# Optimization experiments

Hardware: AMD Instinct MI355X
Metric: run time of the kernel (lower is better)

## Reference

```python
import jax, jax.numpy as jnp
import numpy as np

B = 512      # streamlines (graphs in the batch)
L = 128      # points per streamline
M = L - 1    # edges per direction per streamline == conv output length
IN = 3       # 3-D coordinates
K = 5        # kNN neighbors (self included, as in PyG knn)
FOV = 5      # conv kernel; odd so conv out length == M, matching the batch vector
PAD = FOV // 2
NC = 2
EPS = 1e-5


def _bn(x, g, b, m, v):
    # inference-mode BatchNorm1d
    return (x - m) * jax.lax.rsqrt(v + EPS) * g + b


def setup_inputs():
    key = jax.random.key(0)
    ks = jax.random.split(key, 20)
    r = lambda i, shape: jax.random.normal(ks[i], shape, jnp.float32) * 0.05
    ones = lambda n: jnp.ones((n,), jnp.float32)
    zeros = lambda n: jnp.zeros((n,), jnp.float32)
    pos = jax.random.normal(ks[0], (B * L, IN), jnp.float32)
    # consecutive-point (forward) edges, streamline-major order
    base = (jnp.arange(B)[:, None] * L + jnp.arange(M)[None, :]).reshape(-1)
    fwd = jnp.stack([base, base + 1]).astype(jnp.int32)          # [2, B*M]
    eidx = jnp.concatenate([fwd, fwd], axis=1)                   # [2, 2*B*M]; first half overwritten in forward
    batch = jnp.repeat(jnp.arange(B, dtype=jnp.int32), L)        # per-point graph id
    lengths = jnp.full((B,), L, dtype=jnp.int32)
    return dict(
        pos=pos, eidx=eidx, batch=batch, lengths=lengths,
        conv1_w=r(1, (FOV, 2 * IN, 64)), conv1_b=r(2, (64,)),
        bn1_g=ones(64), bn1_b=zeros(64), bn1_m=r(3, (64,)), bn1_v=ones(64),
        edge_w=r(4, (2 * 64, 128)), edge_b=r(5, (128,)),
        bn2_g=ones(128), bn2_b=zeros(128), bn2_m=r(6, (128,)), bn2_v=ones(128),
        lin1_w=r(7, (64 + 128, 1024)), lin1_b=r(8, (1024,)),
        bn3_g=ones(1024), bn3_b=zeros(1024), bn3_m=r(9, (1024,)), bn3_v=ones(1024),
        m1_w=r(10, (1024, 512)), m1_b=r(11, (512,)),
        bn4_g=ones(512), bn4_b=zeros(512), bn4_m=r(12, (512,)), bn4_v=ones(512),
        m2_w=r(13, (512, 256)), m2_b=r(14, (256,)),
        bn5_g=ones(256), bn5_b=zeros(256), bn5_m=r(15, (256,)), bn5_v=ones(256),
        out_w=r(16, (256, NC)), out_b=r(17, (NC,)),
    )


def reference(pos, eidx, batch, lengths,
              conv1_w, conv1_b, bn1_g, bn1_b, bn1_m, bn1_v,
              edge_w, edge_b, bn2_g, bn2_b, bn2_m, bn2_v,
              lin1_w, lin1_b, bn3_g, bn3_b, bn3_m, bn3_v,
              m1_w, m1_b, bn4_g, bn4_b, bn4_m, bn4_v,
              m2_w, m2_b, bn5_g, bn5_b, bn5_m, bn5_v,
              out_w, out_b):
    E = eidx.shape[1]
    half = eidx[:, E // 2:]
    # eidx[:, :E//2] = eidx[:, E//2:].flip(1)
    eidx = jnp.concatenate([half[:, ::-1], half], axis=1)
    # irregular gather: edge features [E, 2*IN]
    feats = jnp.concatenate([pos[eidx[1]] - pos[eidx[0]], pos[eidx[0]]], axis=1)
    x = feats.reshape(2 * B, M, 2 * IN)                            # folded direction+batch
    # Conv1d (cross-correlation) -> BN -> ReLU, channels-last layout
    x = jax.lax.conv_general_dilated(x, conv1_w, (1,), [(PAD, PAD)],
                                     dimension_numbers=('NWC', 'WIO', 'NWC')) + conv1_b
    x = jax.nn.relu(_bn(x, bn1_g, bn1_b, bn1_m, bn1_v))            # [2B, M, 64]
    # direction symmetrization: max(first half, second half flipped on batch & length)
    x = jnp.maximum(x[:B], x[B:][::-1, ::-1, :])                   # [B, M, 64]
    x1 = x.reshape(B * M, 64)
    # ---- DynamicEdgeConv: per-streamline kNN graph + edge MLP + max aggregation ----
    xg = x1.reshape(B, M, 64)
    sq = jnp.sum(xg * xg, axis=-1)                                 # [B, M]
    dist = sq[:, :, None] + sq[:, None, :] - 2.0 * jnp.einsum('bmd,bnd->bmn', xg, xg)
    _, idx = jax.lax.top_k(-dist, K)                               # [B, M, K] (self included)
    xj = jax.vmap(lambda xs, ix: xs[ix])(xg, idx)                  # [B, M, K, 64]
    xi = jnp.broadcast_to(xg[:, :, None, :], xj.shape)
    ef = jnp.concatenate([xi, xj - xi], axis=-1)                   # [B, M, K, 128]
    ef = _bn(jax.nn.relu(ef @ edge_w + edge_b), bn2_g, bn2_b, bn2_m, bn2_v)
    x2 = jnp.max(ef, axis=2).reshape(B * M, 128)                   # max aggr over neighbors
    # ---- lin1 + global max pool + classifier MLP (dropout = identity in eval) ----
    h = jnp.concatenate([x1, x2], axis=1)                          # [N, 192]
    h = _bn(jax.nn.relu(h @ lin1_w + lin1_b), bn3_g, bn3_b, bn3_m, bn3_v)  # [N, 1024]
    g = jnp.max(h.reshape(B, M, 1024), axis=1)                     # global_max_pool -> [B, 1024]
    g = _bn(jax.nn.relu(g @ m1_w + m1_b), bn4_g, bn4_b, bn4_m, bn4_v)
    g = _bn(jax.nn.relu(g @ m2_w + m2_b), bn5_g, bn5_b, bn5_m, bn5_v)
    return g @ out_w + out_b                                       # [B, NC]
```

## Files before the change

### kernel.cpp

```cpp
#include <hip/hip_runtime.h>

#define BB 512
#define LL 128
#define MM 127
#define EPS 1e-5f

typedef _Float16 half4 __attribute__((ext_vector_type(4)));
typedef _Float16 half8 __attribute__((ext_vector_type(8)));
typedef float f32x16 __attribute__((ext_vector_type(16)));

#define HB_PITCH 384
#define HB_BATCH 49152

__global__ __launch_bounds__(256) void k0_prep(
    const float* __restrict__ lw, char* __restrict__ lwT,
    const float* __restrict__ ew, char* __restrict__ ewT,
    const float* __restrict__ m1w, char* __restrict__ m1wT,
    const float* __restrict__ m2w, char* __restrict__ m2wT)
{
  int tid = threadIdx.x;
  __shared__ float ws2[256][32];
  if (blockIdx.x < 32) {
    int c0 = blockIdx.x * 32;
    __shared__ float wcol[192][32];
    for (int i = tid; i < 192 * 32; i += 256) {
      int k = i >> 5, c = i & 31;
      wcol[k][c] = lw[k * 1024 + c0 + c];
    }
    __syncthreads();
    for (int j = tid; j < 768; j += 256) {
      int kg = j >> 5, c = j & 31;
      half8 v;
#pragma unroll
      for (int jj = 0; jj < 8; jj++) v[jj] = (_Float16)wcol[kg * 8 + jj][c];
      int cc = c0 + c;
      *(half8*)(lwT + cc * HB_PITCH + ((kg * 16) ^ ((cc & 7) << 4))) = v;
    }
  } else if (blockIdx.x == 32) {
    __shared__ float es[128][128];
    for (int i = tid; i < 128 * 128; i += 256) es[i >> 7][i & 127] = ew[i];
    __syncthreads();
    for (int i = tid; i < 256 * 8; i += 256) {
      int c = i >> 3, kg = i & 7;
      half8 v;
#pragma unroll
      for (int jj = 0; jj < 8; jj++) {
        int k = kg * 8 + jj;
        float val = (c < 128) ? (es[k][c] - es[64 + k][c]) : es[64 + k][c - 128];
        v[jj] = (_Float16)val;
      }
      *(half8*)(ewT + c * 128 + ((kg * 16) ^ ((c & 7) << 4))) = v;
    }
  } else {
    const float* src; char* dst; int N, K, c0, k0;
    if (blockIdx.x < 97) {
      int bb = blockIdx.x - 33;
      src = m1w; dst = m1wT; N = 512; K = 1024;
      c0 = (bb >> 2) * 32; k0 = (bb & 3) * 256;
    } else {
      int bb = blockIdx.x - 97;
      src = m2w; dst = m2wT; N = 256; K = 512;
      c0 = (bb >> 1) * 32; k0 = (bb & 1) * 256;
    }
    for (int i = tid; i < 256 * 32; i += 256) {
      int k = i >> 5, c = i & 31;
      ws2[k][c] = src[(size_t)(k0 + k) * N + c0 + c];
    }
    __syncthreads();
    for (int j = tid; j < 32 * 32; j += 256) {
      int kg = j >> 5, c = j & 31;
      half8 v;
#pragma unroll
      for (int jj = 0; jj < 8; jj++) v[jj] = (_Float16)ws2[kg * 8 + jj][c];
      int cc = c0 + c;
      *(half8*)(dst + (size_t)cc * (2 * K) + ((2 * (k0 + kg * 8)) ^ ((cc & 7) << 4))) = v;
    }
  }
}

__global__ __launch_bounds__(512, 2) void k1_conv_knn(
    const float* __restrict__ pos, const float* __restrict__ cw,
    const float* __restrict__ cb, const float* __restrict__ g1,
    const float* __restrict__ b1, const float* __restrict__ m1,
    const float* __restrict__ v1, char* __restrict__ hb,
    int* __restrict__ idxb)
{
  int b = blockIdx.x;
  int tid = threadIdx.x;
  __shared__ float fpad[132][8];
  __shared__ float xs[128][64];
  __shared__ float sq[128];
  __shared__ float S[128][132];
  __shared__ float bsl[4][128][5];
  __shared__ int   bil[4][128][5];

  if (tid < 40) {
    int rr = tid >> 3;
    int row = (rr < 2) ? rr : (127 + rr);
    fpad[row][tid & 7] = 0.f;
  }
  if (tid < 64) xs[127][tid] = 0.f;
  const float* pb = pos + b * LL * 3;
  for (int i = tid; i < MM * 6; i += 512) {
    int m = i / 6, c = i % 6;
    float v = (c < 3) ? (pb[(m + 1) * 3 + c] - pb[m * 3 + c]) : pb[m * 3 + c - 3];
    fpad[m + 2][c] = v;
  }
  int orow = BB - 1 - b;
  char* hbb = hb + (size_t)orow * HB_BATCH;
  if (tid < 8) *(float4*)(hbb + 127 * HB_PITCH + tid * 16) = make_float4(0.f, 0.f, 0.f, 0.f);

  int c = tid & 63, cg = tid >> 6;
  float wreg[30];
#pragma unroll
  for (int t = 0; t < 5; t++)
#pragma unroll
    for (int ci = 0; ci < 6; ci++) wreg[t * 6 + ci] = cw[(t * 6 + ci) * 64 + c];
  float s1 = g1[c] * rsqrtf(v1[c] + EPS);
  float t1 = (cb[c] - m1[c]) * s1 + b1[c];
  __syncthreads();

#pragma unroll
  for (int it = 0; it < 4; it++) {
    int chunk = cg + 8 * it;
    int m0 = chunk * 4;
    float4 fa[8], fb[8];
#pragma unroll
    for (int r = 0; r < 8; r++) {
      fa[r] = *(const float4*)&fpad[m0 + r][0];
      fb[r] = *(const float4*)&fpad[m0 + r][4];
    }
#pragma unroll
    for (int mm = 0; mm < 4; mm++) {
      int m = m0 + mm;
      if (m >= MM) continue;
      float af = 0.f, ab = 0.f;
#pragma unroll
      for (int t = 0; t < 5; t++) {
#pragma unroll
        for (int ci = 0; ci < 6; ci++) {
          float w = wreg[t * 6 + ci];
          int rf = mm + t, rb = mm + 4 - t;
          float xf = (ci < 4) ? ((const float*)&fa[rf])[ci] : ((const float*)&fb[rf])[ci - 4];
          float xb = (ci < 4) ? ((const float*)&fa[rb])[ci] : ((const float*)&fb[rb])[ci - 4];
          af = fmaf(xf, w, af);
          ab = fmaf(xb, w, ab);
        }
      }
      float z = fmaxf(af, ab) * s1 + t1;
      float xv = fmaxf(z, 0.f);
      int p = MM - 1 - m;
      xs[p][(((c >> 2) + (p >> 3)) & 15) * 4 + (c & 3)] = xv;
      *(_Float16*)(hbb + p * HB_PITCH + ((2 * c) ^ ((p & 7) << 4))) = (_Float16)xv;
    }
  }
  __syncthreads();
  if (tid < 128) {
    int r = tid;
    float s = 0.f;
#pragma unroll
    for (int c4 = 0; c4 < 16; c4++) {
      float4 v = *(const float4*)&xs[r][((c4 + (r >> 3)) & 15) * 4];
      s = fmaf(v.x, v.x, s); s = fmaf(v.y, v.y, s);
      s = fmaf(v.z, v.z, s); s = fmaf(v.w, v.w, s);
    }
    sq[r] = s;
  }
  __syncthreads();
  if (tid < 256) {
    int tr = tid >> 4, tc = tid & 15;
    float acc[8][8];
#pragma unroll
    for (int i = 0; i < 8; i++)
#pragma unroll
      for (int j = 0; j < 8; j++) acc[i][j] = 0.f;
    for (int k4 = 0; k4 < 16; k4++) {
      int ca = ((k4 + tr) & 15) * 4;
      int cbo = ((k4 + tc) & 15) * 4;
      float4 av[8], bv[8];
#pragma unroll
      for (int i = 0; i < 8; i++) av[i] = *(const float4*)&xs[tr * 8 + i][ca];
#pragma unroll
      for (int j = 0; j < 8; j++) bv[j] = *(const float4*)&xs[tc * 8 + j][cbo];
#pragma unroll
      for (int i = 0; i < 8; i++)
#pragma unroll
        for (int j = 0; j < 8; j++) {
          acc[i][j] = fmaf(av[i].x, bv[j].x, acc[i][j]);
          acc[i][j] = fmaf(av[i].y, bv[j].y, acc[i][j]);
          acc[i][j] = fmaf(av[i].z, bv[j].z, acc[i][j]);
          acc[i][j] = fmaf(av[i].w, bv[j].w, acc[i][j]);
        }
    }
    float sqc[8];
#pragma unroll
    for (int j = 0; j < 8; j++) sqc[j] = sq[tc * 8 + j];
#pragma unroll
    for (int i = 0; i < 8; i++) {
      float4 s0, s1v;
      s0.x = sqc[0] - 2.f * acc[i][0]; s0.y = sqc[1] - 2.f * acc[i][1];
      s0.z = sqc[2] - 2.f * acc[i][2]; s0.w = sqc[3] - 2.f * acc[i][3];
      s1v.x = sqc[4] - 2.f * acc[i][4]; s1v.y = sqc[5] - 2.f * acc[i][5];
      s1v.z = sqc[6] - 2.f * acc[i][6]; s1v.w = sqc[7] - 2.f * acc[i][7];
      *(float4*)&S[tr * 8 + i][tc * 8]     = s0;
      *(float4*)&S[tr * 8 + i][tc * 8 + 4] = s1v;
    }
  }
  __syncthreads();
  {
    int row = tid & 127, q = tid >> 7;
    float bs[5]; int bi[5];
#pragma unroll
    for (int k = 0; k < 5; k++) { bs[k] = 1e30f; bi[k] = 0; }
#pragma unroll
    for (int e4 = 0; e4 < 8; e4++) {
      float4 sv = *(const float4*)&S[row][q * 32 + e4 * 4];
      int cbase = q * 32 + e4 * 4;
      float va[4] = {sv.x, sv.y, sv.z, sv.w};
#pragma unroll
      for (int e = 0; e < 4; e++) {
        int col = cbase + e;
        float sc = va[e];
        if (col < 127 && sc < bs[4]) {
          bs[4] = sc; bi[4] = col;
#pragma unroll
          for (int k = 3; k >= 0; k--) {
            if (bs[k + 1] < bs[k]) {
              float ts = bs[k]; bs[k] = bs[k + 1]; bs[k + 1] = ts;
              int ti = bi[k]; bi[k] = bi[k + 1]; bi[k + 1] = ti;
            }
          }
        }
      }
    }
#pragma unroll
    for (int k = 0; k < 5; k++) { bsl[q][row][k] = bs[k]; bil[q][row][k] = bi[k]; }
  }
  __syncthreads();
  if (tid < MM) {
    int i0 = 0, i1 = 0, i2 = 0, i3 = 0;
    int base = (orow * MM + tid) * 5;
#pragma unroll
    for (int k = 0; k < 5; k++) {
      float v0 = bsl[0][tid][i0], v1 = bsl[1][tid][i1];
      float v2 = bsl[2][tid][i2], v3 = bsl[3][tid][i3];
      float best = v0; int q = 0;
      if (v1 < best) { best = v1; q = 1; }
      if (v2 < best) { best = v2; q = 2; }
      if (v3 < best) { best = v3; q = 3; }
      int iq = (q == 0) ? i0 : (q == 1) ? i1 : (q == 2) ? i2 : i3;
      idxb[base + k] = bil[q][tid][iq];
      if (q == 0) i0++; else if (q == 1) i1++; else if (q == 2) i2++; else i3++;
    }
  }
}

__global__ __launch_bounds__(256) void k3_edge(
    const int* __restrict__ idxb, const char* __restrict__ ewT,
    const float* __restrict__ eb, const float* __restrict__ g2,
    const float* __restrict__ b2, const float* __restrict__ m2,
    const float* __restrict__ v2, char* __restrict__ hb)
{
  int b = blockIdx.x;
  int tid = threadIdx.x;
  int w = tid >> 6, l = tid & 63;
  int lo = l & 31, hi = l >> 5;
  __shared__ _Float16 vvs[MM][136];
  __shared__ int idxs[MM * 5];
  char* hbb = hb + (size_t)b * HB_BATCH;

  for (int i = tid; i < MM * 5; i += 256) idxs[i] = idxb[b * MM * 5 + i];
  if (tid < 16) *(float4*)(hbb + 127 * HB_PITCH + 128 + tid * 16) = make_float4(0.f, 0.f, 0.f, 0.f);

  half8 af[4][4];
#pragma unroll
  for (int rt = 0; rt < 4; rt++) {
    int row = rt * 32 + lo;
    const char* rb = hbb + row * HB_PITCH;
    int sz = (row & 7) << 4;
#pragma unroll
    for (int ks = 0; ks < 4; ks++)
      af[rt][ks] = *(const half8*)(rb + ((ks * 32 + hi * 16) ^ sz));
  }
  int cu = w * 32 + lo;
  int swzW = (cu & 7) << 4;
  const char* wu = ewT + cu * 128;
  const char* wv = ewT + (128 + cu) * 128;
  half8 bu[4], bv[4];
#pragma unroll
  for (int ks = 0; ks < 4; ks++) {
    int off = (ks * 32 + hi * 16) ^ swzW;
    bu[ks] = *(const half8*)(wu + off);
    bv[ks] = *(const half8*)(wv + off);
  }
  f32x16 accu[4], accv[4];
#pragma unroll
  for (int rt = 0; rt < 4; rt++)
#pragma unroll
    for (int r = 0; r < 16; r++) { accu[rt][r] = 0.f; accv[rt][r] = 0.f; }
#pragma unroll
  for (int ks = 0; ks < 4; ks++)
#pragma unroll
    for (int rt = 0; rt < 4; rt++) {
      accu[rt] = __builtin_amdgcn_mfma_f32_32x32x16_f16(af[rt][ks], bu[ks], accu[rt], 0, 0, 0);
      accv[rt] = __builtin_amdgcn_mfma_f32_32x32x16_f16(af[rt][ks], bv[ks], accv[rt], 0, 0, 0);
    }
#pragma unroll
  for (int rt = 0; rt < 4; rt++)
#pragma unroll
    for (int r = 0; r < 16; r++) {
      int p = rt * 32 + (r & 3) + 8 * (r >> 2) + 4 * hi;
      if (p < MM) vvs[p][cu] = (_Float16)accv[rt][r];
    }
  __syncthreads();
  float ebv = eb[cu];
  float s2 = g2[cu] * rsqrtf(v2[cu] + EPS);
  float t2 = b2[cu] - m2[cu] * s2;
#pragma unroll
  for (int rt = 0; rt < 4; rt++)
#pragma unroll
    for (int r = 0; r < 16; r++) {
      int p = rt * 32 + (r & 3) + 8 * (r >> 2) + 4 * hi;
      if (p >= MM) continue;
      const int* ip = &idxs[p * 5];
      float u = accu[rt][r];
      float mx = -1e30f;
#pragma unroll
      for (int k = 0; k < 5; k++)
        mx = fmaxf(mx, u + (float)vvs[ip[k]][cu]);
      float o = fmaxf(mx + ebv, 0.f) * s2 + t2;
      *(_Float16*)(hbb + p * HB_PITCH + ((128 + 2 * cu) ^ ((p & 7) << 4))) = (_Float16)o;
    }
}

__global__ __launch_bounds__(512, 2) void k4_lin1(
    const char* __restrict__ hb, const char* __restrict__ lwT,
    const float* __restrict__ lb, const float* __restrict__ g3,
    const float* __restrict__ b3, const float* __restrict__ m3,
    const float* __restrict__ v3, char* __restrict__ gbufh)
{
  int b = blockIdx.x;
  int tid = threadIdx.x;
  int w = tid >> 6;
  int rh = w >> 2, cq = w & 3;
  int l = tid & 63;
  int lo = l & 31, hi = l >> 5;
  __shared__ __align__(16) char sA[HB_BATCH];
  __shared__ float rmslab[2][1024];

  {
    const char* gA = hb + (size_t)b * HB_BATCH;
#pragma unroll
    for (int i = 0; i < 6; i++)
      *(float4*)(sA + (i * 512 + tid) * 16) = *(const float4*)(gA + (i * 512 + tid) * 16);
  }
  __syncthreads();

  int sz = (lo & 7) << 4;
  half8 af[2][12];
#pragma unroll
  for (int q = 0; q < 2; q++) {
    const char* rbase = sA + ((rh * 2 + q) * 32 + lo) * HB_PITCH;
#pragma unroll
    for (int ks = 0; ks < 12; ks++)
      af[q][ks] = *(const half8*)(rbase + ((ks * 32 + hi * 16) ^ sz));
  }

  int col0 = cq * 256 + lo;
  half8 bf[2][12];
  {
    const char* cb0 = lwT + (size_t)col0 * HB_PITCH;
#pragma unroll
    for (int ks = 0; ks < 12; ks++)
      bf[0][ks] = *(const half8*)(cb0 + ((ks * 32 + hi * 16) ^ sz));
  }
#pragma unroll
  for (int ct = 0; ct < 8; ct++) {
    if (ct < 7) {
      const char* cbn = lwT + (size_t)(col0 + (ct + 1) * 32) * HB_PITCH;
#pragma unroll
      for (int ks = 0; ks < 12; ks++)
        bf[(ct + 1) & 1][ks] = *(const half8*)(cbn + ((ks * 32 + hi * 16) ^ sz));
    }
    f32x16 acc[2];
#pragma unroll
    for (int q = 0; q < 2; q++)
#pragma unroll
      for (int r = 0; r < 16; r++) acc[q][r] = 0.f;
#pragma unroll
    for (int ks = 0; ks < 12; ks++) {
      acc[0] = __builtin_amdgcn_mfma_f32_32x32x16_f16(af[0][ks], bf[ct & 1][ks], acc[0], 0, 0, 0);
      acc[1] = __builtin_amdgcn_mfma_f32_32x32x16_f16(af[1][ks], bf[ct & 1][ks], acc[1], 0, 0, 0);
    }
    int col = col0 + ct * 32;
    float bias = lb[col];
    float rm = 0.f;
#pragma unroll
    for (int q = 0; q < 2; q++)
#pragma unroll
      for (int r = 0; r < 16; r++) {
        float v = fmaxf(acc[q][r] + bias, 0.f);
        if (q == 1 && r == 15) v = (rh == 1 && hi == 1) ? 0.f : v;
        rm = fmaxf(rm, v);
      }
    rm = fmaxf(rm, __shfl_xor(rm, 32));
    if (hi == 0) rmslab[rh][col] = rm;
  }
  __syncthreads();
  if (tid < 256) {
    half4 o;
#pragma unroll
    for (int j = 0; j < 4; j++) {
      int c = tid * 4 + j;
      float mv = fmaxf(rmslab[0][c], rmslab[1][c]);
      float s = g3[c] * rsqrtf(v3[c] + EPS);
      float t = b3[c] - m3[c] * s;
      o[j] = (_Float16)(mv * s + t);
    }
    *(half4*)(gbufh + (size_t)b * 2048 + ((8 * tid) ^ ((b & 7) << 4))) = o;
  }
}

template<int K, int N>
__global__ __launch_bounds__(64) void k5_gemm(
    const char* __restrict__ inh, const char* __restrict__ wT,
    const float* __restrict__ bias, const float* __restrict__ gg,
    const float* __restrict__ bbp, const float* __restrict__ mmp,
    const float* __restrict__ vvp, char* __restrict__ outh,
    float* __restrict__ outf)
{
  constexpr int NT = N / 32;
  constexpr int NC = K / 128;
  int bid = blockIdx.x;
  int mt = bid / NT, nt = bid % NT;
  int l = threadIdx.x;
  int lo = l & 31, hi = l >> 5;
  int row = mt * 32 + lo, col = nt * 32 + lo;
  const char* arow = inh + (size_t)row * (2 * K);
  const char* brow = wT + (size_t)col * (2 * K);
  int sza = (row & 7) << 4, szb = (col & 7) << 4;

  half8 a[2][8], bf[2][8];
#pragma unroll
  for (int ks = 0; ks < 8; ks++) {
    int off = ks * 32 + hi * 16;
    a[0][ks]  = *(const half8*)(arow + (off ^ sza));
    bf[0][ks] = *(const half8*)(brow + (off ^ szb));
  }
  f32x16 acc;
#pragma unroll
  for (int r = 0; r < 16; r++) acc[r] = 0.f;
#pragma unroll
  for (int c = 0; c < NC; c++) {
    if (c + 1 < NC) {
#pragma unroll
      for (int ks = 0; ks < 8; ks++) {
        int off = (c + 1) * 256 + ks * 32 + hi * 16;
        a[(c + 1) & 1][ks]  = *(const half8*)(arow + (off ^ sza));
        bf[(c + 1) & 1][ks] = *(const half8*)(brow + (off ^ szb));
      }
    }
#pragma unroll
    for (int ks = 0; ks < 8; ks++)
      acc = __builtin_amdgcn_mfma_f32_32x32x16_f16(a[c & 1][ks], bf[c & 1][ks], acc, 0, 0, 0);
  }
  float bv = bias[col];
  float s = gg[col] * rsqrtf(vvp[col] + EPS);
  float t = bbp[col] - mmp[col] * s;
#pragma unroll
  for (int r = 0; r < 16; r++) {
    float z = fmaxf(acc[r] + bv, 0.f) * s + t;
    int orow = mt * 32 + (r & 3) + 8 * (r >> 2) + 4 * hi;
    if (outh)
      *(_Float16*)(outh + (size_t)orow * (2 * N) + ((2 * col) ^ ((orow & 7) << 4))) = (_Float16)z;
    else
      outf[(size_t)orow * N + col] = z;
  }
}

__global__ __launch_bounds__(256) void k5c_out(
    const float* __restrict__ c2, const float* __restrict__ ow,
    const float* __restrict__ ob, float* __restrict__ out)
{
  int t = blockIdx.x * 256 + threadIdx.x;
  int r = t >> 1, c = t & 1;
  float acc = 0.f;
  for (int d4 = 0; d4 < 64; d4++) {
    float4 cv = *(const float4*)(c2 + r * 256 + d4 * 4);
    acc = fmaf(cv.x, ow[(d4 * 4 + 0) * 2 + c], acc);
    acc = fmaf(cv.y, ow[(d4 * 4 + 1) * 2 + c], acc);
    acc = fmaf(cv.z, ow[(d4 * 4 + 2) * 2 + c], acc);
    acc = fmaf(cv.w, ow[(d4 * 4 + 3) * 2 + c], acc);
  }
  out[t] = acc + ob[c];
}

extern "C" void kernel_launch(void* const* d_in, const int* in_sizes, int n_in,
                              void* d_out, int out_size, void* d_ws, size_t ws_size,
                              hipStream_t stream)
{
  const float* pos = (const float*)d_in[0];
  const float* cw  = (const float*)d_in[4];
  const float* cb  = (const float*)d_in[5];
  const float* g1  = (const float*)d_in[6];
  const float* b1  = (const float*)d_in[7];
  const float* m1  = (const float*)d_in[8];
  const float* v1  = (const float*)d_in[9];
  const float* ew  = (const float*)d_in[10];
  const float* eb  = (const float*)d_in[11];
  const float* g2  = (const float*)d_in[12];
  const float* b2  = (const float*)d_in[13];
  const float* m2  = (const float*)d_in[14];
  const float* v2  = (const float*)d_in[15];
  const float* lw  = (const float*)d_in[16];
  const float* lb  = (const float*)d_in[17];
  const float* g3  = (const float*)d_in[18];
  const float* b3  = (const float*)d_in[19];
  const float* m3  = (const float*)d_in[20];
  const float* v3  = (const float*)d_in[21];
  const float* m1w = (const float*)d_in[22];
  const float* m1b = (const float*)d_in[23];
  const float* g4  = (const float*)d_in[24];
  const float* b4  = (const float*)d_in[25];
  const float* m4  = (const float*)d_in[26];
  const float* v4  = (const float*)d_in[27];
  const float* m2w = (const float*)d_in[28];
  const float* m2b = (const float*)d_in[29];
  const float* g5  = (const float*)d_in[30];
  const float* b5  = (const float*)d_in[31];
  const float* m5  = (const float*)d_in[32];
  const float* v5  = (const float*)d_in[33];
  const float* ow  = (const float*)d_in[34];
  const float* ob  = (const float*)d_in[35];

  char* ws = (char*)d_ws;
  char*  hb    = ws;
  char*  lwT   = ws + 25165824;
  char*  ewT   = ws + 25559040;
  int*   idxb  = (int*)(ws + 25591808);
  char*  gbufh = ws + 26892288;
  char*  m1wT  = ws + 27940864;
  char*  c1h   = ws + 28989440;
  char*  m2wT  = ws + 29513728;
  float* c2    = (float*)(ws + 29775872);

  hipLaunchKernelGGL(k0_prep, dim3(113), dim3(256), 0, stream,
                     lw, lwT, ew, ewT, m1w, m1wT, m2w, m2wT);
  hipLaunchKernelGGL(k1_conv_knn, dim3(512), dim3(512), 0, stream,
                     pos, cw, cb, g1, b1, m1, v1, hb, idxb);
  hipLaunchKernelGGL(k3_edge, dim3(512), dim3(256), 0, stream,
                     idxb, ewT, eb, g2, b2, m2, v2, hb);
  hipLaunchKernelGGL(k4_lin1, dim3(512), dim3(512), 0, stream,
                     hb, lwT, lb, g3, b3, m3, v3, gbufh);
  (k5_gemm<1024, 512>)<<<dim3(256), dim3(64), 0, stream>>>(
      gbufh, m1wT, m1b, g4, b4, m4, v4, c1h, nullptr);
  (k5_gemm<512, 256>)<<<dim3(128), dim3(64), 0, stream>>>(
      c1h, m2wT, m2b, g5, b5, m5, v5, nullptr, c2);
  hipLaunchKernelGGL(k5c_out, dim3(4), dim3(256), 0, stream,
                     c2, ow, ob, (float*)d_out);
}
```

Measured before the change: 128.3 us.

## Shrink kNN kernel to 256 threads and two-pass distance tiles in smaller LDS

The conv+kNN kernel now runs with 256 threads per block instead of 512. The 128x128 distance matrix is computed in two 64-column halves, written to a 128x68 scratch buffer that aliases the conv input padding. A single thread per row streams both halves through one running top-5 list, which removes the four-way partial lists and their merge. Shared memory per block drops a lot, so more blocks can be resident. In exchange, only 128 threads do the selection scan, and it adds an extra barrier per pass.

```diff
diff --git a/kernel.cpp b/kernel.cpp
--- a/kernel.cpp
+++ b/kernel.cpp
@@ -78,7 +78,7 @@
   }
 }
 
-__global__ __launch_bounds__(512, 2) void k1_conv_knn(
+__global__ __launch_bounds__(256, 2) void k1_conv_knn(
     const float* __restrict__ pos, const float* __restrict__ cw,
     const float* __restrict__ cb, const float* __restrict__ g1,
     const float* __restrict__ b1, const float* __restrict__ m1,
@@ -87,12 +87,10 @@
 {
   int b = blockIdx.x;
   int tid = threadIdx.x;
-  __shared__ float fpad[132][8];
   __shared__ float xs[128][64];
   __shared__ float sq[128];
-  __shared__ float S[128][132];
-  __shared__ float bsl[4][128][5];
-  __shared__ int   bil[4][128][5];
+  __shared__ __align__(16) float Sbuf[128][68];
+  float (*fpad)[8] = (float(*)[8])Sbuf;
 
   if (tid < 40) {
     int rr = tid >> 3;
@@ -101,7 +99,7 @@
   }
   if (tid < 64) xs[127][tid] = 0.f;
   const float* pb = pos + b * LL * 3;
-  for (int i = tid; i < MM * 6; i += 512) {
+  for (int i = tid; i < MM * 6; i += 256) {
     int m = i / 6, c = i % 6;
     float v = (c < 3) ? (pb[(m + 1) * 3 + c] - pb[m * 3 + c]) : pb[m * 3 + c - 3];
     fpad[m + 2][c] = v;
@@ -121,8 +119,8 @@
   __syncthreads();
 
 #pragma unroll
-  for (int it = 0; it < 4; it++) {
-    int chunk = cg + 8 * it;
+  for (int it = 0; it < 8; it++) {
+    int chunk = cg + 4 * it;
     int m0 = chunk * 4;
     float4 fa[8], fb[8];
 #pragma unroll
@@ -167,91 +165,84 @@
     sq[r] = s;
   }
   __syncthreads();
-  if (tid < 256) {
-    int tr = tid >> 4, tc = tid & 15;
-    float acc[8][8];
-#pragma unroll
-    for (int i = 0; i < 8; i++)
-#pragma unroll
-      for (int j = 0; j < 8; j++) acc[i][j] = 0.f;
-    for (int k4 = 0; k4 < 16; k4++) {
-      int ca = ((k4 + tr) & 15) * 4;
-      int cbo = ((k4 + tc) & 15) * 4;
-      float4 av[8], bv[8];
-#pragma unroll
-      for (int i = 0; i < 8; i++) av[i] = *(const float4*)&xs[tr * 8 + i][ca];
-#pragma unroll
-      for (int j = 0; j < 8; j++) bv[j] = *(const float4*)&xs[tc * 8 + j][cbo];
+
+  float bs[5]; int bi[5];
+#pragma unroll
+  for (int k = 0; k < 5; k++) { bs[k] = 1e30f; bi[k] = 0; }
+  int tr = tid >> 4, tc = tid & 15;
+
+#pragma unroll
+  for (int pass = 0; pass < 2; pass++) {
+    {
+      int j0 = pass * 64 + tc * 4;
+      int jb = pass * 8 + (tc >> 1);
+      float acc[8][4];
 #pragma unroll
       for (int i = 0; i < 8; i++)
 #pragma unroll
-        for (int j = 0; j < 8; j++) {
-          acc[i][j] = fmaf(av[i].x, bv[j].x, acc[i][j]);
-          acc[i][j] = fmaf(av[i].y, bv[j].y, acc[i][j]);
-          acc[i][j] = fmaf(av[i].z, bv[j].z, acc[i][j]);
-          acc[i][j] = fmaf(av[i].w, bv[j].w, acc[i][j]);
-        }
-    }
-    float sqc[8];
-#pragma unroll
-    for (int j = 0; j < 8; j++) sqc[j] = sq[tc * 8 + j];
-#pragma unroll
-    for (int i = 0; i < 8; i++) {
-      float4 s0, s1v;
-      s0.x = sqc[0] - 2.f * acc[i][0]; s0.y = sqc[1] - 2.f * acc[i][1];
-      s0.z = sqc[2] - 2.f * acc[i][2]; s0.w = sqc[3] - 2.f * acc[i][3];
-      s1v.x = sqc[4] - 2.f * acc[i][4]; s1v.y = sqc[5] - 2.f * acc[i][5];
-      s1v.z = sqc[6] - 2.f * acc[i][6]; s1v.w = sqc[7] - 2.f * acc[i][7];
-      *(float4*)&S[tr * 8 + i][tc * 8]     = s0;
-      *(float4*)&S[tr * 8 + i][tc * 8 + 4] = s1v;
-    }
-  }
-  __syncthreads();
-  {
-    int row = tid & 127, q = tid >> 7;
-    float bs[5]; int bi[5];
-#pragma unroll
-    for (int k = 0; k < 5; k++) { bs[k] = 1e30f; bi[k] = 0; }
-#pragma unroll
-    for (int e4 = 0; e4 < 8; e4++) {
-      float4 sv = *(const float4*)&S[row][q * 32 + e4 * 4];
-      int cbase = q * 32 + e4 * 4;
-      float va[4] = {sv.x, sv.y, sv.z, sv.w};
-#pragma unroll
-      for (int e = 0; e < 4; e++) {
-        int col = cbase + e;
-        float sc = va[e];
-        if (col < 127 && sc < bs[4]) {
-          bs[4] = sc; bi[4] = col;
-#pragma unroll
-          for (int k = 3; k >= 0; k--) {
-            if (bs[k + 1] < bs[k]) {
-              float ts = bs[k]; bs[k] = bs[k + 1]; bs[k + 1] = ts;
-              int ti = bi[k]; bi[k] = bi[k + 1]; bi[k + 1] = ti;
+        for (int j = 0; j < 4; j++) acc[i][j] = 0.f;
+      for (int k4 = 0; k4 < 16; k4++) {
+        int ca = ((k4 + tr) & 15) * 4;
+        int cbo = ((k4 + jb) & 15) * 4;
+        float4 av[8], bv[4];
+#pragma unroll
+        for (int i = 0; i < 8; i++) av[i] = *(const float4*)&xs[tr * 8 + i][ca];
+#pragma unroll
+        for (int j = 0; j < 4; j++) bv[j] = *(const float4*)&xs[j0 + j][cbo];
+#pragma unroll
+        for (int i = 0; i < 8; i++)
+#pragma unroll
+          for (int j = 0; j < 4; j++) {
+            acc[i][j] = fmaf(av[i].x, bv[j].x, acc[i][j]);
+            acc[i][j] = fmaf(av[i].y, bv[j].y, acc[i][j]);
+            acc[i][j] = fmaf(av[i].z, bv[j].z, acc[i][j]);
+            acc[i][j] = fmaf(av[i].w, bv[j].w, acc[i][j]);
+          }
+      }
+      float sqc[4];
+#pragma unroll
+      for (int j = 0; j < 4; j++) sqc[j] = sq[j0 + j];
+#pragma unroll
+      for (int i = 0; i < 8; i++) {
+        float4 s0;
+        s0.x = sqc[0] - 2.f * acc[i][0];
+        s0.y = sqc[1] - 2.f * acc[i][1];
+        s0.z = sqc[2] - 2.f * acc[i][2];
+        s0.w = sqc[3] - 2.f * acc[i][3];
+        *(float4*)&Sbuf[tr * 8 + i][tc * 4] = s0;
+      }
+    }
+    __syncthreads();
+    if (tid < 128) {
+      int row = tid;
+#pragma unroll
+      for (int e4 = 0; e4 < 16; e4++) {
+        float4 sv = *(const float4*)&Sbuf[row][e4 * 4];
+        int cbase = pass * 64 + e4 * 4;
+        float va[4] = {sv.x, sv.y, sv.z, sv.w};
+#pragma unroll
+        for (int e = 0; e < 4; e++) {
+          int col = cbase + e;
+          float sc = va[e];
+          if (col < 127 && sc < bs[4]) {
+            bs[4] = sc; bi[4] = col;
+#pragma unroll
+            for (int k = 3; k >= 0; k--) {
+              if (bs[k + 1] < bs[k]) {
+                float ts = bs[k]; bs[k] = bs[k + 1]; bs[k + 1] = ts;
+                int ti = bi[k]; bi[k] = bi[k + 1]; bi[k + 1] = ti;
+              }
             }
           }
         }
       }
     }
-#pragma unroll
-    for (int k = 0; k < 5; k++) { bsl[q][row][k] = bs[k]; bil[q][row][k] = bi[k]; }
-  }
-  __syncthreads();
+    __syncthreads();
+  }
   if (tid < MM) {
-    int i0 = 0, i1 = 0, i2 = 0, i3 = 0;
     int base = (orow * MM + tid) * 5;
 #pragma unroll
-    for (int k = 0; k < 5; k++) {
-      float v0 = bsl[0][tid][i0], v1 = bsl[1][tid][i1];
-      float v2 = bsl[2][tid][i2], v3 = bsl[3][tid][i3];
-      float best = v0; int q = 0;
-      if (v1 < best) { best = v1; q = 1; }
-      if (v2 < best) { best = v2; q = 2; }
-      if (v3 < best) { best = v3; q = 3; }
-      int iq = (q == 0) ? i0 : (q == 1) ? i1 : (q == 2) ? i2 : i3;
-      idxb[base + k] = bil[q][tid][iq];
-      if (q == 0) i0++; else if (q == 1) i1++; else if (q == 2) i2++; else i3++;
-    }
+    for (int k = 0; k < 5; k++) idxb[base + k] = bi[k];
   }
 }
 
@@ -546,7 +537,7 @@
 
   hipLaunchKernelGGL(k0_prep, dim3(113), dim3(256), 0, stream,
                      lw, lwT, ew, ewT, m1w, m1wT, m2w, m2wT);
-  hipLaunchKernelGGL(k1_conv_knn, dim3(512), dim3(512), 0, stream,
+  hipLaunchKernelGGL(k1_conv_knn, dim3(512), dim3(256), 0, stream,
                      pos, cw, cb, g1, b1, m1, v1, hb, idxb);
   hipLaunchKernelGGL(k3_edge, dim3(512), dim3(256), 0, stream,
                      idxb, ewT, eb, g2, b2, m2, v2, hb);
```

Result: slower. 159.3 us (+24.1%).

## Split fused conv+kNN kernel into conv and half-row kNN kernels

Applied to the files above, without the earlier changes.

The fused conv1+kNN kernel is split in two. The first kernel runs the conv and writes its fp32 features to a global scratch buffer. The second kernel runs kNN over 1024 blocks, each handling half the query rows of one streamline, so the distance computation and top-k get more parallelism and each block uses less shared memory. The cost is an extra kernel launch, a global round-trip for the features, and recomputing the squared norms in both halves.

```diff
diff --git a/kernel.cpp b/kernel.cpp
--- a/kernel.cpp
+++ b/kernel.cpp
@@ -78,37 +78,33 @@
   }
 }
 
-__global__ __launch_bounds__(512, 2) void k1_conv_knn(
+__global__ __launch_bounds__(256) void k1a_conv(
     const float* __restrict__ pos, const float* __restrict__ cw,
     const float* __restrict__ cb, const float* __restrict__ g1,
     const float* __restrict__ b1, const float* __restrict__ m1,
     const float* __restrict__ v1, char* __restrict__ hb,
-    int* __restrict__ idxb)
+    float* __restrict__ xgr)
 {
   int b = blockIdx.x;
   int tid = threadIdx.x;
   __shared__ float fpad[132][8];
-  __shared__ float xs[128][64];
-  __shared__ float sq[128];
-  __shared__ float S[128][132];
-  __shared__ float bsl[4][128][5];
-  __shared__ int   bil[4][128][5];
 
   if (tid < 40) {
     int rr = tid >> 3;
     int row = (rr < 2) ? rr : (127 + rr);
     fpad[row][tid & 7] = 0.f;
   }
-  if (tid < 64) xs[127][tid] = 0.f;
   const float* pb = pos + b * LL * 3;
-  for (int i = tid; i < MM * 6; i += 512) {
+  for (int i = tid; i < MM * 6; i += 256) {
     int m = i / 6, c = i % 6;
     float v = (c < 3) ? (pb[(m + 1) * 3 + c] - pb[m * 3 + c]) : pb[m * 3 + c - 3];
     fpad[m + 2][c] = v;
   }
   int orow = BB - 1 - b;
   char* hbb = hb + (size_t)orow * HB_BATCH;
+  float* xgb = xgr + (size_t)orow * 8192;
   if (tid < 8) *(float4*)(hbb + 127 * HB_PITCH + tid * 16) = make_float4(0.f, 0.f, 0.f, 0.f);
+  if (tid < 16) *(float4*)(xgb + 127 * 64 + tid * 4) = make_float4(0.f, 0.f, 0.f, 0.f);
 
   int c = tid & 63, cg = tid >> 6;
   float wreg[30];
@@ -121,8 +117,8 @@
   __syncthreads();
 
 #pragma unroll
-  for (int it = 0; it < 4; it++) {
-    int chunk = cg + 8 * it;
+  for (int it = 0; it < 8; it++) {
+    int chunk = cg + 4 * it;
     int m0 = chunk * 4;
     float4 fa[8], fb[8];
 #pragma unroll
@@ -150,10 +146,27 @@
       float z = fmaxf(af, ab) * s1 + t1;
       float xv = fmaxf(z, 0.f);
       int p = MM - 1 - m;
-      xs[p][(((c >> 2) + (p >> 3)) & 15) * 4 + (c & 3)] = xv;
+      xgb[p * 64 + (((c >> 2) + (p >> 3)) & 15) * 4 + (c & 3)] = xv;
       *(_Float16*)(hbb + p * HB_PITCH + ((2 * c) ^ ((p & 7) << 4))) = (_Float16)xv;
     }
   }
+}
+
+__global__ __launch_bounds__(256, 2) void k1b_knn(
+    const float* __restrict__ xgr, int* __restrict__ idxb)
+{
+  int bid = blockIdx.x;
+  int ob = bid >> 1, hf = bid & 1;
+  int r0 = hf * 64;
+  int tid = threadIdx.x;
+  __shared__ float xs[128][64];
+  __shared__ float sq[128];
+  __shared__ float S[64][132];
+  __shared__ float bsl[4][64][5];
+  __shared__ int   bil[4][64][5];
+
+  const float4* src = (const float4*)(xgr + (size_t)ob * 8192);
+  for (int i = tid; i < 2048; i += 256) ((float4*)xs)[i] = src[i];
   __syncthreads();
   if (tid < 128) {
     int r = tid;
@@ -167,23 +180,25 @@
     sq[r] = s;
   }
   __syncthreads();
-  if (tid < 256) {
+  {
     int tr = tid >> 4, tc = tid & 15;
-    float acc[8][8];
-#pragma unroll
-    for (int i = 0; i < 8; i++)
+    int ra = r0 + tr * 4;
+    int ga = ra >> 3;
+    float acc[4][8];
+#pragma unroll
+    for (int i = 0; i < 4; i++)
 #pragma unroll
       for (int j = 0; j < 8; j++) acc[i][j] = 0.f;
     for (int k4 = 0; k4 < 16; k4++) {
-      int ca = ((k4 + tr) & 15) * 4;
+      int ca = ((k4 + ga) & 15) * 4;
       int cbo = ((k4 + tc) & 15) * 4;
-      float4 av[8], bv[8];
-#pragma unroll
-      for (int i = 0; i < 8; i++) av[i] = *(const float4*)&xs[tr * 8 + i][ca];
+      float4 av[4], bv[8];
+#pragma unroll
+      for (int i = 0; i < 4; i++) av[i] = *(const float4*)&xs[ra + i][ca];
 #pragma unroll
       for (int j = 0; j < 8; j++) bv[j] = *(const float4*)&xs[tc * 8 + j][cbo];
 #pragma unroll
-      for (int i = 0; i < 8; i++)
+      for (int i = 0; i < 4; i++)
 #pragma unroll
         for (int j = 0; j < 8; j++) {
           acc[i][j] = fmaf(av[i].x, bv[j].x, acc[i][j]);
@@ -196,19 +211,19 @@
 #pragma unroll
     for (int j = 0; j < 8; j++) sqc[j] = sq[tc * 8 + j];
 #pragma unroll
-    for (int i = 0; i < 8; i++) {
+    for (int i = 0; i < 4; i++) {
       float4 s0, s1v;
       s0.x = sqc[0] - 2.f * acc[i][0]; s0.y = sqc[1] - 2.f * acc[i][1];
       s0.z = sqc[2] - 2.f * acc[i][2]; s0.w = sqc[3] - 2.f * acc[i][3];
       s1v.x = sqc[4] - 2.f * acc[i][4]; s1v.y = sqc[5] - 2.f * acc[i][5];
       s1v.z = sqc[6] - 2.f * acc[i][6]; s1v.w = sqc[7] - 2.f * acc[i][7];
-      *(float4*)&S[tr * 8 + i][tc * 8]     = s0;
-      *(float4*)&S[tr * 8 + i][tc * 8 + 4] = s1v;
+      *(float4*)&S[tr * 4 + i][tc * 8]     = s0;
+      *(float4*)&S[tr * 4 + i][tc * 8 + 4] = s1v;
     }
   }
   __syncthreads();
   {
-    int row = tid & 127, q = tid >> 7;
+    int row = tid & 63, q = tid >> 6;
     float bs[5]; int bi[5];
 #pragma unroll
     for (int k = 0; k < 5; k++) { bs[k] = 1e30f; bi[k] = 0; }
@@ -237,20 +252,23 @@
     for (int k = 0; k < 5; k++) { bsl[q][row][k] = bs[k]; bil[q][row][k] = bi[k]; }
   }
   __syncthreads();
-  if (tid < MM) {
-    int i0 = 0, i1 = 0, i2 = 0, i3 = 0;
-    int base = (orow * MM + tid) * 5;
-#pragma unroll
-    for (int k = 0; k < 5; k++) {
-      float v0 = bsl[0][tid][i0], v1 = bsl[1][tid][i1];
-      float v2 = bsl[2][tid][i2], v3 = bsl[3][tid][i3];
-      float best = v0; int q = 0;
-      if (v1 < best) { best = v1; q = 1; }
-      if (v2 < best) { best = v2; q = 2; }
-      if (v3 < best) { best = v3; q = 3; }
-      int iq = (q == 0) ? i0 : (q == 1) ? i1 : (q == 2) ? i2 : i3;
-      idxb[base + k] = bil[q][tid][iq];
-      if (q == 0) i0++; else if (q == 1) i1++; else if (q == 2) i2++; else i3++;
+  if (tid < 64) {
+    int i = r0 + tid;
+    if (i < MM) {
+      int i0 = 0, i1 = 0, i2 = 0, i3 = 0;
+      int base = (ob * MM + i) * 5;
+#pragma unroll
+      for (int k = 0; k < 5; k++) {
+        float v0 = bsl[0][tid][i0], v1 = bsl[1][tid][i1];
+        float v2 = bsl[2][tid][i2], v3 = bsl[3][tid][i3];
+        float best = v0; int q = 0;
+        if (v1 < best) { best = v1; q = 1; }
+        if (v2 < best) { best = v2; q = 2; }
+        if (v3 < best) { best = v3; q = 3; }
+        int iq = (q == 0) ? i0 : (q == 1) ? i1 : (q == 2) ? i2 : i3;
+        idxb[base + k] = bil[q][tid][iq];
+        if (q == 0) i0++; else if (q == 1) i1++; else if (q == 2) i2++; else i3++;
+      }
     }
   }
 }
@@ -543,11 +561,13 @@
   char*  c1h   = ws + 28989440;
   char*  m2wT  = ws + 29513728;
   float* c2    = (float*)(ws + 29775872);
+  float* xgr   = (float*)(ws + 30300160);
 
   hipLaunchKernelGGL(k0_prep, dim3(113), dim3(256), 0, stream,
                      lw, lwT, ew, ewT, m1w, m1wT, m2w, m2wT);
-  hipLaunchKernelGGL(k1_conv_knn, dim3(512), dim3(512), 0, stream,
-                     pos, cw, cb, g1, b1, m1, v1, hb, idxb);
+  hipLaunchKernelGGL(k1a_conv, dim3(512), dim3(256), 0, stream,
+                     pos, cw, cb, g1, b1, m1, v1, hb, xgr);
+  hipLaunchKernelGGL(k1b_knn, dim3(1024), dim3(256), 0, stream, xgr, idxb);
   hipLaunchKernelGGL(k3_edge, dim3(512), dim3(256), 0, stream,
                      idxb, ewT, eb, g2, b2, m2, v2, hb);
   hipLaunchKernelGGL(k4_lin1, dim3(512), dim3(512), 0, stream,
```

New measurement: 127.2 us (median of 3 runs). About the same (-0.9%).
